# Kernel optimization log

Measured on AMD Instinct MI355X. Metric: run time of the kernel, lower is better.

## Reference

```python
import jax, jax.numpy as jnp
import numpy as np


def setup_inputs() -> dict:
    key = jax.random.key(0)
    ks = jax.random.split(key, 14)
    n, c, m, s = 32, 256, 32, 64
    rn = lambda k, shape, sc=1.0: jax.random.normal(k, shape, dtype=jnp.float32) * sc
    return {
        "seg_ori": rn(ks[0], (n, c, m, m)),
        "edge_ori": rn(ks[1], (n, c, m, m)),
        "W_s1": rn(ks[2], (s, c), 0.05), "b_s1": rn(ks[3], (s,), 0.05),
        "W_s11": rn(ks[4], (s, c), 0.05), "b_s11": rn(ks[5], (s,), 0.05),
        "W_mlp": rn(ks[6], (s, c), 0.05), "b_mlp": rn(ks[7], (s,), 0.05),
        "w_s2": rn(ks[8], ()), "b_s2": rn(ks[9], ()),
        "w_s3": rn(ks[10], ()), "b_s3": rn(ks[11], ()),
        "W_g": rn(ks[12], (c, c), 0.02), "b_g": rn(ks[13], (c,), 0.02),
    }


def reference(seg_ori, edge_ori, W_s1, b_s1, W_s11, b_s11, W_mlp, b_mlp,
              w_s2, b_s2, w_s3, b_s3, W_g, b_g):
    n, c, m, _ = seg_ori.shape
    hw = m * m                      # num_n = mids^2
    s = W_s1.shape[0]               # num_s = plane_mid
    seg = seg_ori

    # ---- channel affinity branch ----
    seg_s = jnp.einsum('nchw,sc->nshw', seg, W_s1) + b_s1[None, :, None, None]
    theta_T = seg_s.reshape(n, s, hw)        # view(n, num_s, -1)
    theta = seg_s.reshape(n, hw, s)          # view(n, -1, num_s): reshape, NOT transpose
    ch_att = jax.nn.relu(jnp.mean(seg, axis=(2, 3)) @ W_mlp.T + b_mlp)   # (n, s)
    diag_c = ch_att[:, :, None] * ch_att[:, None, :]                     # (n, s, s) outer
    sim_c = jnp.einsum('nps,nst->npt', theta, diag_c)                    # (n, hw, s)
    sim_c = jax.nn.softmax(jnp.einsum('npt,ntq->npq', sim_c, theta_T), axis=1)  # (n, hw, hw)

    # ---- spatial affinity branch ----
    seg_c = jnp.einsum('nchw,sc->nshw', seg, W_s11) + b_s11[None, :, None, None]
    sigma = seg_c.reshape(n, s, hw)
    sigma_T = seg_c.reshape(n, hw, s)
    sigma_out = jnp.einsum('nps,nsq->npq', sigma_T, sigma)               # (n, hw, hw)
    edge_m = seg * edge_ori
    maxpool_s = jnp.max(seg, axis=1)                                     # (n, m, m)
    edge_m_pool = jnp.max(edge_m, axis=1)                                # (n, m, m)
    seg_ss = (maxpool_s * w_s2 + b_s2).reshape(n, 1, hw)                 # 1x1 conv, 1 channel
    edge_mm = (edge_m_pool * w_s3 + b_s3).reshape(n, hw, 1)
    sim_s = jax.nn.softmax(edge_mm * seg_ss * sigma_out, axis=1)         # (n, hw, hw)

    similarity = sim_c + sim_s

    # ---- GCN: bmm + conv1d(k=1) + relu + residual ----
    seg2 = seg.reshape(n, c, hw)
    seg_sim = jnp.einsum('ncp,npq->ncq', seg2, similarity)               # (n, c, hw)
    out = jax.nn.relu(jnp.einsum('ncl,oc->nol', seg_sim, W_g) + b_g[None, :, None])
    gcn_out = (out + seg2).reshape(n, c, m, m)
    return gcn_out + seg_ori
```

## Files before the change

### kernel.cpp

```cpp
#include <hip/hip_runtime.h>

#define N 32
#define C 256
#define HW 1024
#define S 64
#define LOG2E 1.4426950408889634f

typedef _Float16 f16;
typedef _Float16 f16x4 __attribute__((ext_vector_type(4)));
typedef _Float16 f16x8 __attribute__((ext_vector_type(8)));
typedef float f32x4 __attribute__((ext_vector_type(4)));

#define MFMA(a, b, c) __builtin_amdgcn_mfma_f32_16x16x32_f16(a, b, c, 0, 0, 0)
#define EXP2(x) exp2f(x)

__device__ inline f16x8 lds_ld8(const f16* p) {
    return *(const f16x8*)p;
}

__global__ void __launch_bounds__(256) k_pool1(const float* seg, const float* edge,
        f16* segf, float* pms, float* pme, float* mean,
        const float* Ws1, const float* Ws11, const float* Wg, f16* Wf, f16* Wgf) {
    int n = blockIdx.x, cg = blockIdx.y;
    int t = threadIdx.x, w = t >> 6, lane = t & 63;
    int flat = n * 32 + cg;
    if (flat < 256) {
        int i = flat * 256 + t;
        if (i < S * C) { Wf[i] = (f16)Ws1[i]; Wf[S * C + i] = (f16)Ws11[i]; }
        Wgf[i] = (f16)Wg[i];
    }
    int p4 = (lane << 2) + (w << 8);
    size_t base = (size_t)n * C * HW;
    float4 ms = make_float4(-3e38f, -3e38f, -3e38f, -3e38f);
    float4 me = ms;
    __shared__ float psum[4][8];
    for (int ci = 0; ci < 8; ci++) {
        int c = cg * 8 + ci;
        size_t off = base + (size_t)c * HW + p4;
        float4 s = *(const float4*)(seg + off);
        float4 e = *(const float4*)(edge + off);
        union { f16 h[4]; unsigned long long u; } pk;
        pk.h[0] = (f16)s.x; pk.h[1] = (f16)s.y; pk.h[2] = (f16)s.z; pk.h[3] = (f16)s.w;
        *(unsigned long long*)(segf + off) = pk.u;
        ms.x = fmaxf(ms.x, s.x); ms.y = fmaxf(ms.y, s.y);
        ms.z = fmaxf(ms.z, s.z); ms.w = fmaxf(ms.w, s.w);
        me.x = fmaxf(me.x, s.x * e.x); me.y = fmaxf(me.y, s.y * e.y);
        me.z = fmaxf(me.z, s.z * e.z); me.w = fmaxf(me.w, s.w * e.w);
        float sm = s.x + s.y + s.z + s.w;
        for (int o = 32; o; o >>= 1) sm += __shfl_down(sm, o);
        if (lane == 0) psum[w][ci] = sm;
    }
    __syncthreads();
    if (t < 8)
        mean[n * C + cg * 8 + t] =
            (psum[0][t] + psum[1][t] + psum[2][t] + psum[3][t]) * (1.0f / HW);
    size_t pb = ((size_t)n * 32 + cg) * HW + p4;
    *(float4*)(pms + pb) = ms;
    *(float4*)(pme + pb) = me;
}

__global__ void __launch_bounds__(256) k_pool2(const float* pms, const float* pme,
        float* a2, float* bq, const float* ws2, const float* bs2,
        const float* ws3, const float* bs3,
        const float* mean, const float* Wmlp, const float* bmlp, float* chat) {
    int n = blockIdx.x, t = threadIdx.x;
    int p4 = t << 2;
    float4 ms = make_float4(-3e38f, -3e38f, -3e38f, -3e38f);
    float4 me = ms;
    for (int cg = 0; cg < 32; cg++) {
        size_t pb = ((size_t)n * 32 + cg) * HW + p4;
        float4 a = *(const float4*)(pms + pb);
        float4 b = *(const float4*)(pme + pb);
        ms.x = fmaxf(ms.x, a.x); ms.y = fmaxf(ms.y, a.y);
        ms.z = fmaxf(ms.z, a.z); ms.w = fmaxf(ms.w, a.w);
        me.x = fmaxf(me.x, b.x); me.y = fmaxf(me.y, b.y);
        me.z = fmaxf(me.z, b.z); me.w = fmaxf(me.w, b.w);
    }
    float w3 = ws3[0], b3 = bs3[0], w2 = ws2[0], b2 = bs2[0];
    float4 av, bv;
    av.x = (me.x * w3 + b3) * LOG2E; av.y = (me.y * w3 + b3) * LOG2E;
    av.z = (me.z * w3 + b3) * LOG2E; av.w = (me.w * w3 + b3) * LOG2E;
    bv.x = ms.x * w2 + b2; bv.y = ms.y * w2 + b2;
    bv.z = ms.z * w2 + b2; bv.w = ms.w * w2 + b2;
    *(float4*)(a2 + (size_t)n * HW + p4) = av;
    *(float4*)(bq + (size_t)n * HW + p4) = bv;
    if (t < S) {
        float acc = 0.f;
        const float* wr = Wmlp + (size_t)t * C;
        for (int c = 0; c < C; c++) acc += mean[n * C + c] * wr[c];
        chat[n * S + t] = fmaxf(acc + bmlp[t], 0.f);
    }
}

__global__ void __launch_bounds__(512) k_proj(const f16* segf, const f16* Wf,
        const float* bs1, const float* bs11, const float* chat,
        f16* segc, float* dp2, float* e_, float* dpmm2) {
    int n = blockIdx.x, qt = blockIdx.y;
    int q0 = qt * 64;
    __shared__ f16 sT[64][264];
    __shared__ f16 pT[64][72];
    __shared__ float cA[S];
    const f16* sb = segf + (size_t)n * C * HW + q0;
    int tid = threadIdx.x;
    if (tid < S) cA[tid] = chat[n * S + tid];
    for (int idx = tid; idx < 2048; idx += 512) {
        int c = idx >> 3, q8 = (idx & 7) << 3;
        f16x8 v = *(const f16x8*)(sb + (size_t)c * HW + q8);
        for (int j = 0; j < 8; j++) sT[q8 + j][c] = v[j];
    }
    __syncthreads();
    int lane = tid & 63, wv = tid >> 6;
    int lm = lane & 15, lg = lane >> 4;
    f32x4 acc[4] = {};
    for (int ck = 0; ck < 8; ck++) {
        int c0 = ck * 32;
        f16x8 a0 = *(const f16x8*)(Wf + (size_t)(wv * 16 + lm) * C + c0 + lg * 8);
        for (int j = 0; j < 4; j++) {
            f16x8 b = lds_ld8(&sT[j * 16 + lm][c0 + lg * 8]);
            acc[j] = MFMA(a0, b, acc[j]);
        }
    }
    for (int rr = 0; rr < 4; rr++) {
        int row = wv * 16 + lg * 4 + rr;
        float bias = (row < S) ? bs1[row] : bs11[row - S];
        for (int j = 0; j < 4; j++) {
            int q = q0 + j * 16 + lm;
            float v = acc[j][rr] + bias;
            if (row < S) pT[row][j * 16 + lm] = (f16)v;
            else         segc[((size_t)n * S + (row - S)) * HW + q] = (f16)v;
        }
    }
    __syncthreads();
    if (tid < 64) {
        float a2c = 0.f;
        for (int t = 0; t < S; t += 8) {
            f16x8 v = lds_ld8(&pT[tid][t]);
            for (int j = 0; j < 8; j++) a2c += (float)v[j] * cA[t + j];
        }
        float d2 = a2c * LOG2E;
        dp2[(size_t)n * HW + 16 * tid + qt] = d2;
        float mx = d2, mn = d2;
        for (int o = 32; o; o >>= 1) {
            mx = fmaxf(mx, __shfl_down(mx, o));
            mn = fminf(mn, __shfl_down(mn, o));
        }
        if (tid == 0) {
            dpmm2[(n * 16 + qt) * 2]     = mx;
            dpmm2[(n * 16 + qt) * 2 + 1] = mn;
        }
    } else if (tid < 128) {
        int ql = tid - 64;
        float a2c = 0.f;
        for (int t = 0; t < S; t++) a2c += cA[t] * (float)pT[t][ql];
        e_[(size_t)n * HW + q0 + ql] = a2c;
    }
}

__global__ void __launch_bounds__(512) k_zs(const f16* segc, const float* a2,
        const float* bq, const float* dp2, const float* e_, const float* dpmm2,
        float* Ms2, float* iZs, float* Mc2, float* iZc) {
    int n = blockIdx.x, q0 = blockIdx.y * 32;
    __shared__ f16 bT[32][72];
    __shared__ float a2s[HW];
    __shared__ float d[HW];
    __shared__ float mred[32][4], lred[32][4];
    const f16* cb = segc + (size_t)n * S * HW;
    int tid = threadIdx.x;
    if (tid < 256) {
        int th = tid >> 2, q8 = (tid & 3) << 3;
        f16x8 v = *(const f16x8*)(cb + (size_t)th * HW + q0 + q8);
        for (int j = 0; j < 8; j++) bT[q8 + j][th] = v[j];
    }
    for (int i = tid; i < HW; i += 512) {
        a2s[i] = a2[(size_t)n * HW + i];
        d[i]   = dp2[(size_t)n * HW + i];
    }
    __syncthreads();
    int w = tid >> 6, lane = tid & 63, lm = lane & 15, lg = lane >> 4;
    int qg = w >> 2, ph = w & 3;
    f16x8 b0 = lds_ld8(&bT[qg * 16 + lm][lg * 8]);
    f16x8 b1 = lds_ld8(&bT[qg * 16 + lm][32 + lg * 8]);
    float bqv = bq[(size_t)n * HW + q0 + qg * 16 + lm];
    float m = -3e38f, l = 0.f;
    for (int it = 0; it < 8; it++) {
        int pb = ph * 256 + it * 32;
        f16x8 a0 = *(const f16x8*)(cb + (size_t)(pb + lm) * S + lg * 8);
        f16x8 a1 = *(const f16x8*)(cb + (size_t)(pb + lm) * S + 32 + lg * 8);
        f16x8 c0 = *(const f16x8*)(cb + (size_t)(pb + 16 + lm) * S + lg * 8);
        f16x8 c1 = *(const f16x8*)(cb + (size_t)(pb + 16 + lm) * S + 32 + lg * 8);
        f32x4 sgA = {}, sgB = {};
        sgA = MFMA(a0, b0, sgA); sgA = MFMA(a1, b1, sgA);
        sgB = MFMA(c0, b0, sgB); sgB = MFMA(c1, b1, sgB);
        float sc[8];
        float fm = -3e38f;
        for (int rr = 0; rr < 4; rr++) {
            float avA = a2s[pb + lg * 4 + rr];
            float avB = a2s[pb + 16 + lg * 4 + rr];
            sc[rr]     = avA * bqv * sgA[rr];
            sc[rr + 4] = avB * bqv * sgB[rr];
            fm = fmaxf(fm, fmaxf(sc[rr], sc[rr + 4]));
        }
        fm = fmaxf(fm, __shfl_xor(fm, 16));
        fm = fmaxf(fm, __shfl_xor(fm, 32));
        float fl = 0.f;
        for (int rr = 0; rr < 8; rr++) fl += EXP2(sc[rr] - fm);
        fl += __shfl_xor(fl, 16);
        fl += __shfl_xor(fl, 32);
        float nm = fmaxf(m, fm);
        l = l * EXP2(m - nm) + fl * EXP2(fm - nm);
        m = nm;
    }
    if (lg == 0) { mred[qg * 16 + lm][ph] = m; lred[qg * 16 + lm][ph] = l; }
    __syncthreads();
    if (tid < 32) {
        float M = fmaxf(fmaxf(mred[tid][0], mred[tid][1]),
                        fmaxf(mred[tid][2], mred[tid][3]));
        float L = lred[tid][0] * EXP2(mred[tid][0] - M)
                + lred[tid][1] * EXP2(mred[tid][1] - M)
                + lred[tid][2] * EXP2(mred[tid][2] - M)
                + lred[tid][3] * EXP2(mred[tid][3] - M);
        Ms2[(size_t)n * HW + q0 + tid] = M;
        iZs[(size_t)n * HW + q0 + tid] = 1.f / L;
    }
    float mx = -3e38f, mn = 3e38f;
    for (int j2 = 0; j2 < 16; j2++) {
        mx = fmaxf(mx, dpmm2[(n * 16 + j2) * 2]);
        mn = fminf(mn, dpmm2[(n * 16 + j2) * 2 + 1]);
    }
    int qz = q0 + (tid >> 4);
    int pi = tid & 15;
    float eq = e_[(size_t)n * HW + qz];
    float mz = (eq > 0.f) ? eq * mx : eq * mn;
    float z = 0.f;
    for (int j2 = 0; j2 < 64; j2++) z += EXP2(d[pi + 16 * j2] * eq - mz);
    z += __shfl_xor(z, 1);
    z += __shfl_xor(z, 2);
    z += __shfl_xor(z, 4);
    z += __shfl_xor(z, 8);
    if (pi == 0) {
        Mc2[(size_t)n * HW + qz] = mz;
        iZc[(size_t)n * HW + qz] = 1.f / z;
    }
}

__global__ void __launch_bounds__(512, 4) k_fused(const f16* segf, const f16* segc,
        const float* dp2, const float* e_, const float* a2, const float* bq,
        const float* Mc2, const float* iZc, const float* Ms2, const float* iZs,
        const f16* Wgf, const float* bg, float* out) {
    int n = blockIdx.x, q0 = blockIdx.y * 64;
    __shared__ f16 bT[64][72];
    __shared__ f16 wT[2][64][136];
    __shared__ float2 da[HW];
    const f16* cb = segc + (size_t)n * S * HW;
    const f16* sb = segf + (size_t)n * C * HW;
    int tid = threadIdx.x;
    for (int idx = tid; idx < 64 * 32; idx += 512) {
        int q = idx & 63, th = (idx >> 6) << 1;
        union { f16 h[2]; unsigned u; } pk;
        pk.h[0] = cb[(size_t)th * HW + q0 + q];
        pk.h[1] = cb[(size_t)(th + 1) * HW + q0 + q];
        *(unsigned*)&bT[q][th] = pk.u;
    }
    for (int i = tid; i < HW; i += 512)
        da[i] = make_float2(dp2[(size_t)n * HW + i], a2[(size_t)n * HW + i]);
    __syncthreads();
    int w = tid >> 6, lane = tid & 63, lm = lane & 15, lg = lane >> 4;
    float ev[4], bqv[4], mcv[4], izcv[4], msv[4], izsv[4];
    for (int j = 0; j < 4; j++) {
        size_t gq = (size_t)n * HW + q0 + j * 16 + lm;
        ev[j] = e_[gq];  bqv[j] = bq[gq];
        mcv[j] = Mc2[gq]; izcv[j] = iZc[gq];
        msv[j] = Ms2[gq]; izsv[j] = iZs[gq];
    }
    f32x4 acc[2][4] = {};
    for (int chk = 0; chk <= 8; chk++) {
        if (chk > 0) {
            int p0 = (chk - 1) * 128;
            int cur = (chk - 1) & 1;
            #pragma unroll
            for (int ks = 0; ks < 4; ks++) {
                f16x8 a2f[2];
                #pragma unroll
                for (int cf = 0; cf < 2; cf++) {
                    int crow = w * 32 + cf * 16 + lm;
                    a2f[cf] = *(const f16x8*)(sb + (size_t)crow * HW + p0 + ks * 32 + lg * 8);
                }
                #pragma unroll
                for (int qf = 0; qf < 4; qf++) {
                    f16x8 bb = lds_ld8(&wT[cur][qf * 16 + lm][ks * 32 + lg * 8]);
                    acc[0][qf] = MFMA(a2f[0], bb, acc[0][qf]);
                    acc[1][qf] = MFMA(a2f[1], bb, acc[1][qf]);
                }
            }
        }
        if (chk < 8) {
            int p0 = chk * 128;
            const f16* sp = cb + (size_t)(p0 + w * 16 + lm) * S;
            f16x8 sa0 = *(const f16x8*)(sp + lg * 8);
            f16x8 sa1 = *(const f16x8*)(sp + 32 + lg * 8);
            float d2r[4], avr[4];
            #pragma unroll
            for (int rr = 0; rr < 4; rr++) {
                float2 dv = da[p0 + w * 16 + lg * 4 + rr];
                d2r[rr] = dv.x; avr[rr] = dv.y;
            }
            #pragma unroll
            for (int j = 0; j < 4; j++) {
                f16x8 bb0 = lds_ld8(&bT[j * 16 + lm][lg * 8]);
                f16x8 bb1 = lds_ld8(&bT[j * 16 + lm][32 + lg * 8]);
                f32x4 sg = {};
                sg = MFMA(sa0, bb0, sg);
                sg = MFMA(sa1, bb1, sg);
                float wgt[4];
                #pragma unroll
                for (int rr = 0; rr < 4; rr++) {
                    float wc  = EXP2(d2r[rr] * ev[j] - mcv[j]) * izcv[j];
                    float wsv = EXP2(avr[rr] * bqv[j] * sg[rr] - msv[j]) * izsv[j];
                    wgt[rr] = wc + wsv;
                }
                int ql = j * 16 + lm;
                int pp = w * 16 + lg * 4;
                union { f16 h[2]; unsigned u; } c0u, c1u;
                c0u.h[0] = (f16)wgt[0]; c0u.h[1] = (f16)wgt[1];
                c1u.h[0] = (f16)wgt[2]; c1u.h[1] = (f16)wgt[3];
                *(unsigned*)&wT[chk & 1][ql][pp]     = c0u.u;
                *(unsigned*)&wT[chk & 1][ql][pp + 2] = c1u.u;
            }
        }
        __syncthreads();
    }
    f16 (*sT2)[264] = (f16(*)[264])&wT[0][0][0];
    for (int cf = 0; cf < 2; cf++)
        for (int qf = 0; qf < 4; qf++) {
            int crow = w * 32 + cf * 16 + lg * 4;
            int ql = qf * 16 + lm;
            f16x4 pk;
            pk[0] = (f16)acc[cf][qf][0]; pk[1] = (f16)acc[cf][qf][1];
            pk[2] = (f16)acc[cf][qf][2]; pk[3] = (f16)acc[cf][qf][3];
            *(f16x4*)&sT2[ql][crow] = pk;
        }
    __syncthreads();
    int ow = w * 32;
    f32x4 acc2[2][4] = {};
    for (int ck = 0; ck < 8; ck++) {
        int c0 = ck * 32;
        f16x8 af0 = *(const f16x8*)(Wgf + (size_t)(ow + lm) * C + c0 + lg * 8);
        f16x8 af1 = *(const f16x8*)(Wgf + (size_t)(ow + 16 + lm) * C + c0 + lg * 8);
        for (int qf = 0; qf < 4; qf++) {
            f16x8 bf = lds_ld8(&sT2[qf * 16 + lm][c0 + lg * 8]);
            acc2[0][qf] = MFMA(af0, bf, acc2[0][qf]);
            acc2[1][qf] = MFMA(af1, bf, acc2[1][qf]);
        }
    }
    for (int of = 0; of < 2; of++)
        for (int rr = 0; rr < 4; rr++) {
            int o = ow + of * 16 + lg * 4 + rr;
            float bgv = bg[o];
            for (int qf = 0; qf < 4; qf++) {
                int q = q0 + qf * 16 + lm;
                size_t ix = ((size_t)n * C + o) * HW + q;
                out[ix] = fmaxf(acc2[of][qf][rr] + bgv, 0.f) + 2.f * (float)sb[((size_t)o * HW) + q];
            }
        }
}

extern "C" void kernel_launch(void* const* d_in, const int* in_sizes, int n_in,
                              void* d_out, int out_size, void* d_ws, size_t ws_size,
                              hipStream_t stream) {
    const float* seg  = (const float*)d_in[0];
    const float* edge = (const float*)d_in[1];
    const float* Ws1  = (const float*)d_in[2];
    const float* bs1  = (const float*)d_in[3];
    const float* Ws11 = (const float*)d_in[4];
    const float* bs11 = (const float*)d_in[5];
    const float* Wmlp = (const float*)d_in[6];
    const float* bmlp = (const float*)d_in[7];
    const float* ws2  = (const float*)d_in[8];
    const float* bs2  = (const float*)d_in[9];
    const float* ws3  = (const float*)d_in[10];
    const float* bs3  = (const float*)d_in[11];
    const float* Wg   = (const float*)d_in[12];
    const float* bg   = (const float*)d_in[13];
    float* out = (float*)d_out;
    char* wsb = (char*)d_ws;

    f16*   segf   = (f16*)(wsb);
    f16*   segc   = (f16*)(wsb + 16777216);
    float* dpmm2  = (float*)(wsb + 20971520);
    float* pms    = (float*)(wsb + 25165824);
    float* pme    = (float*)(wsb + 29360128);
    f16*   Wf     = (f16*)(wsb + 41943040);
    f16*   Wgf    = (f16*)(wsb + 42008576);
    float* mean   = (float*)(wsb + 42139648);
    float* chat   = (float*)(wsb + 42172416);
    float* dp2    = (float*)(wsb + 42180608);
    float* e_     = (float*)(wsb + 42311680);
    float* a2     = (float*)(wsb + 42442752);
    float* bq     = (float*)(wsb + 42573824);
    float* Mc2    = (float*)(wsb + 42704896);
    float* iZc    = (float*)(wsb + 42835968);
    float* Ms2    = (float*)(wsb + 42967040);
    float* iZs    = (float*)(wsb + 43098112);

    k_pool1<<<dim3(32, 32), 256, 0, stream>>>(seg, edge, segf, pms, pme, mean,
                                              Ws1, Ws11, Wg, Wf, Wgf);
    k_pool2<<<32, 256, 0, stream>>>(pms, pme, a2, bq, ws2, bs2, ws3, bs3,
                                    mean, Wmlp, bmlp, chat);
    k_proj<<<dim3(32, 16), 512, 0, stream>>>(segf, Wf, bs1, bs11, chat,
                                             segc, dp2, e_, dpmm2);
    k_zs<<<dim3(32, 32), 512, 0, stream>>>(segc, a2, bq, dp2, e_, dpmm2,
                                           Ms2, iZs, Mc2, iZc);
    k_fused<<<dim3(32, 16), 512, 0, stream>>>(segf, segc, dp2, e_, a2, bq,
                                              Mc2, iZc, Ms2, iZs, Wgf, bg, out);
}
```

Measured before the change: 245.0 us.

## Fuse softmax normalizer computation into main fused kernel, drop k_zs launch

Removes the separate k_zs kernel and computes the spatial-softmax max/sum and the channel-softmax normalizers inside k_fused, using the segc tile and the dp2/a2 data already staged in shared memory. This eliminates one launch and the global round trip for the four normalizer arrays. The cost is that k_fused now does the extra MFMA/exp prologue per block before its main loop, which adds shared memory and registers. It may reduce occupancy and lengthen the critical path of the heaviest kernel.

Result: faster. 228.9 us (-6.6%).

```diff
diff --git a/kernel.cpp b/kernel.cpp
--- a/kernel.cpp
+++ b/kernel.cpp
@@ -156,101 +156,15 @@
     }
 }
 
-__global__ void __launch_bounds__(512) k_zs(const f16* segc, const float* a2,
-        const float* bq, const float* dp2, const float* e_, const float* dpmm2,
-        float* Ms2, float* iZs, float* Mc2, float* iZc) {
-    int n = blockIdx.x, q0 = blockIdx.y * 32;
-    __shared__ f16 bT[32][72];
-    __shared__ float a2s[HW];
-    __shared__ float d[HW];
-    __shared__ float mred[32][4], lred[32][4];
-    const f16* cb = segc + (size_t)n * S * HW;
-    int tid = threadIdx.x;
-    if (tid < 256) {
-        int th = tid >> 2, q8 = (tid & 3) << 3;
-        f16x8 v = *(const f16x8*)(cb + (size_t)th * HW + q0 + q8);
-        for (int j = 0; j < 8; j++) bT[q8 + j][th] = v[j];
-    }
-    for (int i = tid; i < HW; i += 512) {
-        a2s[i] = a2[(size_t)n * HW + i];
-        d[i]   = dp2[(size_t)n * HW + i];
-    }
-    __syncthreads();
-    int w = tid >> 6, lane = tid & 63, lm = lane & 15, lg = lane >> 4;
-    int qg = w >> 2, ph = w & 3;
-    f16x8 b0 = lds_ld8(&bT[qg * 16 + lm][lg * 8]);
-    f16x8 b1 = lds_ld8(&bT[qg * 16 + lm][32 + lg * 8]);
-    float bqv = bq[(size_t)n * HW + q0 + qg * 16 + lm];
-    float m = -3e38f, l = 0.f;
-    for (int it = 0; it < 8; it++) {
-        int pb = ph * 256 + it * 32;
-        f16x8 a0 = *(const f16x8*)(cb + (size_t)(pb + lm) * S + lg * 8);
-        f16x8 a1 = *(const f16x8*)(cb + (size_t)(pb + lm) * S + 32 + lg * 8);
-        f16x8 c0 = *(const f16x8*)(cb + (size_t)(pb + 16 + lm) * S + lg * 8);
-        f16x8 c1 = *(const f16x8*)(cb + (size_t)(pb + 16 + lm) * S + 32 + lg * 8);
-        f32x4 sgA = {}, sgB = {};
-        sgA = MFMA(a0, b0, sgA); sgA = MFMA(a1, b1, sgA);
-        sgB = MFMA(c0, b0, sgB); sgB = MFMA(c1, b1, sgB);
-        float sc[8];
-        float fm = -3e38f;
-        for (int rr = 0; rr < 4; rr++) {
-            float avA = a2s[pb + lg * 4 + rr];
-            float avB = a2s[pb + 16 + lg * 4 + rr];
-            sc[rr]     = avA * bqv * sgA[rr];
-            sc[rr + 4] = avB * bqv * sgB[rr];
-            fm = fmaxf(fm, fmaxf(sc[rr], sc[rr + 4]));
-        }
-        fm = fmaxf(fm, __shfl_xor(fm, 16));
-        fm = fmaxf(fm, __shfl_xor(fm, 32));
-        float fl = 0.f;
-        for (int rr = 0; rr < 8; rr++) fl += EXP2(sc[rr] - fm);
-        fl += __shfl_xor(fl, 16);
-        fl += __shfl_xor(fl, 32);
-        float nm = fmaxf(m, fm);
-        l = l * EXP2(m - nm) + fl * EXP2(fm - nm);
-        m = nm;
-    }
-    if (lg == 0) { mred[qg * 16 + lm][ph] = m; lred[qg * 16 + lm][ph] = l; }
-    __syncthreads();
-    if (tid < 32) {
-        float M = fmaxf(fmaxf(mred[tid][0], mred[tid][1]),
-                        fmaxf(mred[tid][2], mred[tid][3]));
-        float L = lred[tid][0] * EXP2(mred[tid][0] - M)
-                + lred[tid][1] * EXP2(mred[tid][1] - M)
-                + lred[tid][2] * EXP2(mred[tid][2] - M)
-                + lred[tid][3] * EXP2(mred[tid][3] - M);
-        Ms2[(size_t)n * HW + q0 + tid] = M;
-        iZs[(size_t)n * HW + q0 + tid] = 1.f / L;
-    }
-    float mx = -3e38f, mn = 3e38f;
-    for (int j2 = 0; j2 < 16; j2++) {
-        mx = fmaxf(mx, dpmm2[(n * 16 + j2) * 2]);
-        mn = fminf(mn, dpmm2[(n * 16 + j2) * 2 + 1]);
-    }
-    int qz = q0 + (tid >> 4);
-    int pi = tid & 15;
-    float eq = e_[(size_t)n * HW + qz];
-    float mz = (eq > 0.f) ? eq * mx : eq * mn;
-    float z = 0.f;
-    for (int j2 = 0; j2 < 64; j2++) z += EXP2(d[pi + 16 * j2] * eq - mz);
-    z += __shfl_xor(z, 1);
-    z += __shfl_xor(z, 2);
-    z += __shfl_xor(z, 4);
-    z += __shfl_xor(z, 8);
-    if (pi == 0) {
-        Mc2[(size_t)n * HW + qz] = mz;
-        iZc[(size_t)n * HW + qz] = 1.f / z;
-    }
-}
-
 __global__ void __launch_bounds__(512, 4) k_fused(const f16* segf, const f16* segc,
         const float* dp2, const float* e_, const float* a2, const float* bq,
-        const float* Mc2, const float* iZc, const float* Ms2, const float* iZs,
-        const f16* Wgf, const float* bg, float* out) {
+        const float* dpmm2, const f16* Wgf, const float* bg, float* out) {
     int n = blockIdx.x, q0 = blockIdx.y * 64;
     __shared__ f16 bT[64][72];
     __shared__ f16 wT[2][64][136];
     __shared__ float2 da[HW];
+    __shared__ float mred[64][9], lred[64][9];
+    __shared__ float msL[64], izsL[64], mcL[64], izcL[64];
     const f16* cb = segc + (size_t)n * S * HW;
     const f16* sb = segf + (size_t)n * C * HW;
     int tid = threadIdx.x;
@@ -265,12 +179,84 @@
         da[i] = make_float2(dp2[(size_t)n * HW + i], a2[(size_t)n * HW + i]);
     __syncthreads();
     int w = tid >> 6, lane = tid & 63, lm = lane & 15, lg = lane >> 4;
-    float ev[4], bqv[4], mcv[4], izcv[4], msv[4], izsv[4];
+    float ev[4], bqv[4];
     for (int j = 0; j < 4; j++) {
         size_t gq = (size_t)n * HW + q0 + j * 16 + lm;
         ev[j] = e_[gq];  bqv[j] = bq[gq];
-        mcv[j] = Mc2[gq]; izcv[j] = iZc[gq];
-        msv[j] = Ms2[gq]; izsv[j] = iZs[gq];
+    }
+    float sm[4], sl[4];
+    #pragma unroll
+    for (int j = 0; j < 4; j++) { sm[j] = -3e38f; sl[j] = 0.f; }
+    for (int chk = 0; chk < 8; chk++) {
+        int p0 = chk * 128;
+        const f16* sp = cb + (size_t)(p0 + w * 16 + lm) * S;
+        f16x8 sa0 = *(const f16x8*)(sp + lg * 8);
+        f16x8 sa1 = *(const f16x8*)(sp + 32 + lg * 8);
+        float avr[4];
+        #pragma unroll
+        for (int rr = 0; rr < 4; rr++) avr[rr] = da[p0 + w * 16 + lg * 4 + rr].y;
+        #pragma unroll
+        for (int j = 0; j < 4; j++) {
+            f16x8 bb0 = lds_ld8(&bT[j * 16 + lm][lg * 8]);
+            f16x8 bb1 = lds_ld8(&bT[j * 16 + lm][32 + lg * 8]);
+            f32x4 sg = {};
+            sg = MFMA(sa0, bb0, sg);
+            sg = MFMA(sa1, bb1, sg);
+            float sc[4], fm = -3e38f;
+            #pragma unroll
+            for (int rr = 0; rr < 4; rr++) {
+                sc[rr] = avr[rr] * bqv[j] * sg[rr];
+                fm = fmaxf(fm, sc[rr]);
+            }
+            fm = fmaxf(fm, __shfl_xor(fm, 16));
+            fm = fmaxf(fm, __shfl_xor(fm, 32));
+            float fl = 0.f;
+            #pragma unroll
+            for (int rr = 0; rr < 4; rr++) fl += EXP2(sc[rr] - fm);
+            fl += __shfl_xor(fl, 16);
+            fl += __shfl_xor(fl, 32);
+            float nm = fmaxf(sm[j], fm);
+            sl[j] = sl[j] * EXP2(sm[j] - nm) + fl * EXP2(fm - nm);
+            sm[j] = nm;
+        }
+    }
+    if (lg == 0)
+        #pragma unroll
+        for (int j = 0; j < 4; j++) {
+            mred[j * 16 + lm][w] = sm[j];
+            lred[j * 16 + lm][w] = sl[j];
+        }
+    {
+        float mx = -3e38f, mn = 3e38f;
+        for (int j2 = 0; j2 < 16; j2++) {
+            mx = fmaxf(mx, dpmm2[(n * 16 + j2) * 2]);
+            mn = fminf(mn, dpmm2[(n * 16 + j2) * 2 + 1]);
+        }
+        int qz = tid >> 3, pi = tid & 7;
+        float eqz = e_[(size_t)n * HW + q0 + qz];
+        float mzv = (eqz > 0.f) ? eqz * mx : eqz * mn;
+        float z = 0.f;
+        for (int j2 = 0; j2 < 128; j2++) z += EXP2(da[pi + 8 * j2].x * eqz - mzv);
+        z += __shfl_xor(z, 1);
+        z += __shfl_xor(z, 2);
+        z += __shfl_xor(z, 4);
+        if (pi == 0) { mcL[qz] = mzv; izcL[qz] = 1.f / z; }
+    }
+    __syncthreads();
+    if (tid < 64) {
+        float M = mred[tid][0];
+        for (int ww = 1; ww < 8; ww++) M = fmaxf(M, mred[tid][ww]);
+        float L = 0.f;
+        for (int ww = 0; ww < 8; ww++) L += lred[tid][ww] * EXP2(mred[tid][ww] - M);
+        msL[tid] = M; izsL[tid] = 1.f / L;
+    }
+    __syncthreads();
+    float mcv[4], izcv[4], msv[4], izsv[4];
+    #pragma unroll
+    for (int j = 0; j < 4; j++) {
+        int q = j * 16 + lm;
+        mcv[j] = mcL[q]; izcv[j] = izcL[q];
+        msv[j] = msL[q]; izsv[j] = izsL[q];
     }
     f32x4 acc[2][4] = {};
     for (int chk = 0; chk <= 8; chk++) {
@@ -397,10 +383,6 @@
     float* e_     = (float*)(wsb + 42311680);
     float* a2     = (float*)(wsb + 42442752);
     float* bq     = (float*)(wsb + 42573824);
-    float* Mc2    = (float*)(wsb + 42704896);
-    float* iZc    = (float*)(wsb + 42835968);
-    float* Ms2    = (float*)(wsb + 42967040);
-    float* iZs    = (float*)(wsb + 43098112);
 
     k_pool1<<<dim3(32, 32), 256, 0, stream>>>(seg, edge, segf, pms, pme, mean,
                                               Ws1, Ws11, Wg, Wf, Wgf);
@@ -408,8 +390,6 @@
                                     mean, Wmlp, bmlp, chat);
     k_proj<<<dim3(32, 16), 512, 0, stream>>>(segf, Wf, bs1, bs11, chat,
                                              segc, dp2, e_, dpmm2);
-    k_zs<<<dim3(32, 32), 512, 0, stream>>>(segc, a2, bq, dp2, e_, dpmm2,
-                                           Ms2, iZs, Mc2, iZc);
     k_fused<<<dim3(32, 16), 512, 0, stream>>>(segf, segc, dp2, e_, a2, bq,
-                                              Mc2, iZc, Ms2, iZs, Wgf, bg, out);
-}
+                                              dpmm2, Wgf, bg, out);
+}
```
